# Optimization experiments

Measured on AMD Instinct MI355X. Metric: run time of the kernel, lower is better.

Reference implementation:

```python
import jax, jax.numpy as jnp
import numpy as np

N_NODES = 50000
N_EDGES = 800000
DIM_IN, DIM_H, DIM_OUT = 96, 128, 16


def setup_inputs() -> dict:
    key = jax.random.key(0)
    ks = jax.random.split(key, 8)
    x = jax.random.normal(ks[0], (N_NODES, DIM_IN), dtype=jnp.float32)
    edge_index = jax.random.randint(ks[1], (2, N_EDGES), 0, N_NODES, dtype=jnp.int64)
    W1_l = jax.random.normal(ks[2], (DIM_IN, DIM_H), dtype=jnp.float32) * 0.1
    b1_l = jax.random.normal(ks[3], (DIM_H,), dtype=jnp.float32) * 0.1
    W1_r = jax.random.normal(ks[4], (DIM_IN, DIM_H), dtype=jnp.float32) * 0.1
    W2_l = jax.random.normal(ks[5], (DIM_H, DIM_OUT), dtype=jnp.float32) * 0.1
    b2_l = jax.random.normal(ks[6], (DIM_OUT,), dtype=jnp.float32) * 0.1
    W2_r = jax.random.normal(ks[7], (DIM_H, DIM_OUT), dtype=jnp.float32) * 0.1
    return {"x": x, "edge_index": edge_index, "W1_l": W1_l, "b1_l": b1_l,
            "W1_r": W1_r, "W2_l": W2_l, "b2_l": b2_l, "W2_r": W2_r}


def _mean_aggregate(x, src, dst, n_nodes):
    # gather neighbor features along edges, mean-reduce at destination nodes
    msgs = x[src]                                      # [E, d]
    agg = jax.ops.segment_sum(msgs, dst, num_segments=n_nodes)  # [N, d]
    deg = jax.ops.segment_sum(jnp.ones_like(src, dtype=x.dtype), dst,
                              num_segments=n_nodes)    # [N]
    return agg / jnp.maximum(deg, 1.0)[:, None]


def _sage_conv(x, src, dst, W_l, b_l, W_r):
    # PyG SAGEConv (mean aggr): lin_l(mean_j x_j) + lin_r(x); bias on lin_l only
    agg = _mean_aggregate(x, src, dst, x.shape[0])
    return agg @ W_l + b_l + x @ W_r


def reference(x, edge_index, W1_l, b1_l, W1_r, W2_l, b2_l, W2_r):
    src, dst = edge_index[0], edge_index[1]
    h = jax.nn.relu(_sage_conv(x, src, dst, W1_l, b1_l, W1_r))
    h = _sage_conv(h, src, dst, W2_l, b2_l, W2_r)
    return jax.nn.softmax(h, axis=1)
```

## Files before the change

kernel.cpp:

```cpp
#include <hip/hip_runtime.h>

#define NN 50000
#define NE 800000
#define DIN 96
#define DH 128
#define DOUT 16
#define NBKT ((NN + 127) / 128)
#define EPB 8192

typedef __attribute__((ext_vector_type(8))) short bf16x8;
typedef __attribute__((ext_vector_type(4))) float f32x4;

__device__ inline short f2bf(float f) {
    unsigned u = __float_as_uint(f);
    u += 0x7fff + ((u >> 16) & 1);
    return (short)(u >> 16);
}
__device__ inline float bflo(unsigned u) { return __uint_as_float(u << 16); }
__device__ inline float bfhi(unsigned u) { return __uint_as_float(u & 0xffff0000u); }

#define XB_BLOCKS ((NN * DIN / 4 + 255) / 256)
#define WC_BLOCKS ((DH * 192 + 32 * DH + 255) / 256)
#define HB_BLOCKS ((NE + 8191) / 8192)
__global__ __launch_bounds__(256) void k_prep(const float* __restrict__ x,
                                              const float* __restrict__ W1l,
                                              const float* __restrict__ W1r,
                                              const float* __restrict__ W2l,
                                              const float* __restrict__ W2r,
                                              const int* __restrict__ ei,
                                              short* __restrict__ xb,
                                              short* __restrict__ Bt,
                                              short* __restrict__ Bt2,
                                              int* __restrict__ bcntg) {
    __shared__ int h[NBKT];
    if (blockIdx.x < XB_BLOCKS) {
        int i = blockIdx.x * 256 + threadIdx.x;
        if (i < NN * DIN / 4) {
            float4 v = ((const float4*)x)[i];
            short4 o;
            o.x = f2bf(v.x); o.y = f2bf(v.y); o.z = f2bf(v.z); o.w = f2bf(v.w);
            ((short4*)xb)[i] = o;
        }
    } else if (blockIdx.x < XB_BLOCKS + WC_BLOCKS) {
        int idx = (blockIdx.x - XB_BLOCKS) * 256 + threadIdx.x;
        if (idx < DH * 192) {
            int n = idx / 192, kk = idx % 192;
            float v = (kk < DIN) ? W1l[kk * DH + n] : W1r[(kk - DIN) * DH + n];
            Bt[idx] = f2bf(v);
        } else if (idx < DH * 192 + 32 * DH) {
            int j = idx - DH * 192;
            int c = j >> 7, k = j & 127;
            float v = (c < DOUT) ? W2l[k * DOUT + c] : W2r[k * DOUT + (c - DOUT)];
            Bt2[j] = f2bf(v);
        }
    } else {
        for (int i = threadIdx.x; i < NBKT; i += 256) h[i] = 0;
        __syncthreads();
        const int base = (blockIdx.x - XB_BLOCKS - WC_BLOCKS) * 8192;
        const int end = min(base + 8192, NE);
        for (int i = base + threadIdx.x; i < end; i += 256)
            atomicAdd(&h[ei[NE + i] >> 7], 1);
        __syncthreads();
        for (int b = threadIdx.x; b < NBKT; b += 256)
            if (h[b]) atomicAdd(&bcntg[b], h[b]);
    }
}

__global__ __launch_bounds__(512) void k_bscan(const int* __restrict__ bcntg,
                                               int* __restrict__ boff, int* __restrict__ gbcur) {
    __shared__ int buf[512];
    const int t = threadIdx.x;
    int v = (t < NBKT) ? bcntg[t] : 0;
    buf[t] = v;
    __syncthreads();
    for (int o = 1; o < 512; o <<= 1) {
        int tv = (t >= o) ? buf[t - o] : 0;
        __syncthreads();
        buf[t] += tv;
        __syncthreads();
    }
    if (t < NBKT) {
        int ex = buf[t] - v;
        boff[t] = ex;
        gbcur[t] = ex;
    }
    if (t == 0) boff[NBKT] = NE;
}

__global__ __launch_bounds__(512) void k_bucket(const int* __restrict__ ei,
                                                int* __restrict__ gbcur,
                                                unsigned* __restrict__ bpack) {
    __shared__ unsigned stage[EPB];
    __shared__ int bcnt[NBKT];
    __shared__ int bfill[NBKT];
    __shared__ int brun[NBKT];
    __shared__ int bres[NBKT];
    __shared__ int sbuf[512];
    const int tid = threadIdx.x;
    const int e0 = blockIdx.x * EPB;
    const int ecnt = min(EPB, NE - e0);

    for (int i = tid; i < NBKT; i += 512) { bcnt[i] = 0; bfill[i] = 0; }
    __syncthreads();
    for (int i = tid; i < ecnt; i += 512)
        atomicAdd(&bcnt[(unsigned)ei[NE + e0 + i] >> 7], 1);
    __syncthreads();
    int v = (tid < NBKT) ? bcnt[tid] : 0;
    sbuf[tid] = v;
    __syncthreads();
    for (int o = 1; o < 512; o <<= 1) {
        int tv = (tid >= o) ? sbuf[tid - o] : 0;
        __syncthreads();
        sbuf[tid] += tv;
        __syncthreads();
    }
    if (tid < NBKT) brun[tid] = sbuf[tid] - v;
    __syncthreads();
    for (int i = tid; i < ecnt; i += 512) {
        unsigned s = (unsigned)ei[e0 + i];
        unsigned d = (unsigned)ei[NE + e0 + i];
        int b = d >> 7;
        int p = atomicAdd(&bfill[b], 1);
        stage[brun[b] + p] = (d << 16) | s;
    }
    __syncthreads();
    for (int b = tid; b < NBKT; b += 512) {
        int n = bcnt[b];
        bres[b] = n ? atomicAdd(&gbcur[b], n) : 0;
    }
    __syncthreads();
    for (int i = tid; i < ecnt; i += 512) {
        unsigned p = stage[i];
        int b = p >> 23;
        bpack[bres[b] + (i - brun[b])] = p;
    }
}

__global__ __launch_bounds__(256) void k_bfill(const unsigned* __restrict__ bpack,
                                               const int* __restrict__ boff,
                                               int* __restrict__ off,
                                               int* __restrict__ csr) {
    __shared__ unsigned stage[4096];
    __shared__ int ncnt[128];
    __shared__ int nrun[128];
    __shared__ int lcur[128];
    __shared__ int buf[256];
    const int b = blockIdx.x;
    const int tid = threadIdx.x;
    const int pb = boff[b], pe = boff[b + 1];
    const int cnt = pe - pb;
    const bool st = (cnt <= 4096);
    if (tid < 128) { ncnt[tid] = 0; lcur[tid] = 0; }
    __syncthreads();
    for (int i = tid; i < cnt; i += 256) {
        unsigned p = bpack[pb + i];
        if (st) stage[i] = p;
        atomicAdd(&ncnt[(p >> 16) & 127], 1);
    }
    __syncthreads();
    int v = (tid < 128) ? ncnt[tid] : 0;
    buf[tid] = v;
    __syncthreads();
    for (int o = 1; o < 128; o <<= 1) {
        int tv = (tid >= o) ? buf[tid - o] : 0;
        __syncthreads();
        buf[tid] += tv;
        __syncthreads();
    }
    if (tid < 128) {
        nrun[tid] = buf[tid] - v;
        const int n = b * 128 + tid;
        if (n <= NN) off[n] = pb + nrun[tid];
    }
    __syncthreads();
    for (int i = tid; i < cnt; i += 256) {
        unsigned p = st ? stage[i] : bpack[pb + i];
        int nd = (p >> 16) & 127;
        int pos = atomicAdd(&lcur[nd], 1);
        csr[pb + nrun[nd] + pos] = (int)(p & 0xffffu);
    }
}

__global__ __launch_bounds__(256) void k_agg1(const short* __restrict__ xb,
                                              const int* __restrict__ csr,
                                              const int* __restrict__ off,
                                              short* __restrict__ m1b) {
    const int w = threadIdx.x >> 6;
    const int l = threadIdx.x & 63;
    const int n = blockIdx.x * 4 + w;
    if (n >= NN) return;
    const int eg = l / 12;
    const int c  = l % 12;
    const int b = off[n], e = off[n + 1];
    const float4* xq = (const float4*)xb;
    float acc[8];
#pragma unroll
    for (int k = 0; k < 8; ++k) acc[k] = 0.f;
    int i = (eg < 4) ? b + eg : e;
    for (; i + 4 < e; i += 8) {
        int s0 = csr[i], s1 = csr[i + 4];
        float4 v0 = xq[(size_t)s0 * 12 + c];
        float4 v1 = xq[(size_t)s1 * 12 + c];
        const unsigned* u0 = (const unsigned*)&v0;
        const unsigned* u1 = (const unsigned*)&v1;
#pragma unroll
        for (int j = 0; j < 4; ++j) {
            acc[2 * j]     += bflo(u0[j]) + bflo(u1[j]);
            acc[2 * j + 1] += bfhi(u0[j]) + bfhi(u1[j]);
        }
    }
    if (i < e) {
        float4 v0 = xq[(size_t)csr[i] * 12 + c];
        const unsigned* u0 = (const unsigned*)&v0;
#pragma unroll
        for (int j = 0; j < 4; ++j) {
            acc[2 * j]     += bflo(u0[j]);
            acc[2 * j + 1] += bfhi(u0[j]);
        }
    }
#pragma unroll
    for (int k = 0; k < 8; ++k) acc[k] += __shfl(acc[k], l + 24);
#pragma unroll
    for (int k = 0; k < 8; ++k) acc[k] += __shfl(acc[k], l + 12);
    if (l < 12) {
        const float inv = (e > b) ? 1.0f / (float)(e - b) : 0.0f;
        uint4 o;
        unsigned* op = (unsigned*)&o;
#pragma unroll
        for (int j = 0; j < 4; ++j)
            op[j] = (unsigned)(unsigned short)f2bf(acc[2 * j] * inv)
                  | ((unsigned)(unsigned short)f2bf(acc[2 * j + 1] * inv) << 16);
        ((uint4*)m1b)[(size_t)n * 12 + l] = o;
    }
}

#define SHP 136
__global__ __launch_bounds__(256) void k_linproj(const short* __restrict__ m1b,
                                                 const short* __restrict__ xb,
                                                 const short* __restrict__ Bt,
                                                 const float* __restrict__ b1,
                                                 const short* __restrict__ Bt2,
                                                 const float* __restrict__ b2,
                                                 short* __restrict__ zlb,
                                                 float* __restrict__ s) {
    __shared__ __align__(16) short sh[64][SHP];
    const int w = threadIdx.x >> 6;
    const int l = threadIdx.x & 63;
    const int lr = l & 15;
    const int lk = l >> 4;
    int row = blockIdx.x * 64 + w * 16 + lr;
    if (row >= NN) row = NN - 1;

    f32x4 acc[8];
#pragma unroll
    for (int nt = 0; nt < 8; ++nt) {
        float bv = b1[nt * 16 + lr];
        acc[nt] = (f32x4){bv, bv, bv, bv};
    }

    bf16x8 afr[6];
    {
        const bf16x8* am = (const bf16x8*)(m1b + (size_t)row * DIN);
        const bf16x8* ax = (const bf16x8*)(xb  + (size_t)row * DIN);
        afr[0] = am[lk];     afr[1] = am[4 + lk]; afr[2] = am[8 + lk];
        afr[3] = ax[lk];     afr[4] = ax[4 + lk]; afr[5] = ax[8 + lk];
    }

    const bf16x8* bt8 = (const bf16x8*)Bt;
#pragma unroll
    for (int st = 0; st < 6; ++st) {
#pragma unroll
        for (int nt = 0; nt < 8; ++nt) {
            bf16x8 bfr = bt8[(size_t)(nt * 16 + lr) * 24 + st * 4 + lk];
            acc[nt] = __builtin_amdgcn_mfma_f32_16x16x32_bf16(afr[st], bfr, acc[nt], 0, 0, 0);
        }
    }

    const int lrow0 = w * 16 + lk * 4;
#pragma unroll
    for (int r = 0; r < 4; ++r) {
#pragma unroll
        for (int nt = 0; nt < 8; ++nt)
            sh[lrow0 + r][nt * 16 + lr] = f2bf(fmaxf(acc[nt][r], 0.f));
    }
    __syncthreads();

    bf16x8 pafr[4];
#pragma unroll
    for (int st = 0; st < 4; ++st)
        pafr[st] = *(const bf16x8*)&sh[w * 16 + lr][st * 32 + lk * 8];

    f32x4 accz = (f32x4){0.f, 0.f, 0.f, 0.f};
    float bv = b2[lr];
    f32x4 accs = (f32x4){bv, bv, bv, bv};
    const bf16x8* b8 = (const bf16x8*)Bt2;
#pragma unroll
    for (int st = 0; st < 4; ++st) {
        bf16x8 bz = b8[(size_t)lr * 16 + st * 4 + lk];
        bf16x8 bs = b8[(size_t)(16 + lr) * 16 + st * 4 + lk];
        accz = __builtin_amdgcn_mfma_f32_16x16x32_bf16(pafr[st], bz, accz, 0, 0, 0);
        accs = __builtin_amdgcn_mfma_f32_16x16x32_bf16(pafr[st], bs, accs, 0, 0, 0);
    }

    const int orow0 = blockIdx.x * 64 + w * 16 + lk * 4;
#pragma unroll
    for (int r = 0; r < 4; ++r) {
        const int orow = orow0 + r;
        if (orow < NN) {
            zlb[(size_t)orow * DOUT + lr] = f2bf(accz[r]);
            s[(size_t)orow * DOUT + lr] = accs[r];
        }
    }
}

__global__ __launch_bounds__(256) void k_agg2(const short* __restrict__ zlb,
                                              const float* __restrict__ s,
                                              const int* __restrict__ csr,
                                              const int* __restrict__ off,
                                              float* __restrict__ out) {
    const int w = threadIdx.x >> 6;
    const int lane = threadIdx.x & 63;
    const int n = blockIdx.x * 4 + w;
    if (n >= NN) return;
    const int b = off[n], e = off[n + 1];
    const int ng = lane >> 2;
    const int sl = lane & 3;
    const uint2* z2 = (const uint2*)zlb;
    float4 acc = {0.f, 0.f, 0.f, 0.f};
    for (int i = b + ng; i < e; i += 16) {
        uint2 u = z2[(size_t)csr[i] * 4 + sl];
        acc.x += bflo(u.x);
        acc.y += bfhi(u.x);
        acc.z += bflo(u.y);
        acc.w += bfhi(u.y);
    }
#pragma unroll
    for (int o = 4; o <= 32; o <<= 1) {
        acc.x += __shfl_xor(acc.x, o);
        acc.y += __shfl_xor(acc.y, o);
        acc.z += __shfl_xor(acc.z, o);
        acc.w += __shfl_xor(acc.w, o);
    }
    const float inv = (e > b) ? 1.0f / (float)(e - b) : 0.0f;
    const float4 sv = ((const float4*)s)[(size_t)n * 4 + sl];
    float4 v;
    v.x = acc.x * inv + sv.x;
    v.y = acc.y * inv + sv.y;
    v.z = acc.z * inv + sv.z;
    v.w = acc.w * inv + sv.w;
    float mx = fmaxf(fmaxf(v.x, v.y), fmaxf(v.z, v.w));
    mx = fmaxf(mx, __shfl_xor(mx, 1));
    mx = fmaxf(mx, __shfl_xor(mx, 2));
    v.x = expf(v.x - mx); v.y = expf(v.y - mx);
    v.z = expf(v.z - mx); v.w = expf(v.w - mx);
    float sm = v.x + v.y + v.z + v.w;
    sm += __shfl_xor(sm, 1);
    sm += __shfl_xor(sm, 2);
    const float r = 1.0f / sm;
    v.x *= r; v.y *= r; v.z *= r; v.w *= r;
    if (ng == 0) ((float4*)out)[(size_t)n * 4 + sl] = v;
}

template <typename T>
static inline T* align_up(void* p, size_t a = 64) {
    return (T*)(((uintptr_t)p + (a - 1)) & ~(uintptr_t)(a - 1));
}

extern "C" void kernel_launch(void* const* d_in, const int* in_sizes, int n_in,
                              void* d_out, int out_size, void* d_ws, size_t ws_size,
                              hipStream_t stream) {
    const float* x   = (const float*)d_in[0];
    const int*   ei  = (const int*)d_in[1];
    const float* W1l = (const float*)d_in[2];
    const float* b1  = (const float*)d_in[3];
    const float* W1r = (const float*)d_in[4];
    const float* W2l = (const float*)d_in[5];
    const float* b2  = (const float*)d_in[6];
    const float* W2r = (const float*)d_in[7];
    float* out = (float*)d_out;

    unsigned* bpack = (unsigned*)d_ws;
    float* s     = (float*)(bpack + NE);
    int* off     = (int*)(s + (size_t)NN * DOUT);
    int* boff    = off + NN + 1;
    int* gbcur   = boff + NBKT + 1;
    int* bcntg   = gbcur + NBKT;
    int* csr     = bcntg + NBKT;
    short* xb    = align_up<short>(csr + NE);
    short* m1b   = xb + (size_t)NN * DIN;
    short* zlb   = m1b + (size_t)NN * DIN;
    short* Bt    = zlb + (size_t)NN * DOUT;
    short* Bt2   = Bt + (size_t)DH * 192;

    hipMemsetAsync(bcntg, 0, NBKT * sizeof(int), stream);

    k_prep<<<XB_BLOCKS + WC_BLOCKS + HB_BLOCKS, 256, 0, stream>>>(
        x, W1l, W1r, W2l, W2r, ei, xb, Bt, Bt2, bcntg);
    k_bscan<<<1, 512, 0, stream>>>(bcntg, boff, gbcur);
    k_bucket<<<(NE + EPB - 1) / EPB, 512, 0, stream>>>(ei, gbcur, bpack);
    k_bfill<<<NBKT, 256, 0, stream>>>(bpack, boff, off, csr);

    k_agg1<<<(NN + 3) / 4, 256, 0, stream>>>(xb, csr, off, m1b);
    k_linproj<<<(NN + 63) / 64, 256, 0, stream>>>(m1b, xb, Bt, b1, Bt2, b2, zlb, s);
    k_agg2<<<(NN + 3) / 4, 256, 0, stream>>>(zlb, s, csr, off, out);
}
```

Before: 127.6 us.

## Replace global bucket histogram and scan with fixed-capacity bucket slots

Drops the global destination histogram pass and the single-block scan kernel by giving each 128-node bucket a fixed-capacity slot in the packed edge buffer. CSR offsets become separate start/end arrays per node. k_bucket also keeps destination indices in registers between its count and scatter passes instead of reloading them. The cost is a capacity bound per bucket that assumes roughly uniform destination degrees; overflowing edges would be lost.

```diff
diff --git a/kernel.cpp b/kernel.cpp
--- a/kernel.cpp
+++ b/kernel.cpp
@@ -6,6 +6,7 @@
 #define DH 128
 #define DOUT 16
 #define NBKT ((NN + 127) / 128)
+#define CAP 2560
 #define EPB 8192
 
 typedef __attribute__((ext_vector_type(8))) short bf16x8;
@@ -21,18 +22,15 @@
 
 #define XB_BLOCKS ((NN * DIN / 4 + 255) / 256)
 #define WC_BLOCKS ((DH * 192 + 32 * DH + 255) / 256)
-#define HB_BLOCKS ((NE + 8191) / 8192)
 __global__ __launch_bounds__(256) void k_prep(const float* __restrict__ x,
                                               const float* __restrict__ W1l,
                                               const float* __restrict__ W1r,
                                               const float* __restrict__ W2l,
                                               const float* __restrict__ W2r,
-                                              const int* __restrict__ ei,
                                               short* __restrict__ xb,
                                               short* __restrict__ Bt,
                                               short* __restrict__ Bt2,
-                                              int* __restrict__ bcntg) {
-    __shared__ int h[NBKT];
+                                              int* __restrict__ gbcur) {
     if (blockIdx.x < XB_BLOCKS) {
         int i = blockIdx.x * 256 + threadIdx.x;
         if (i < NN * DIN / 4) {
@@ -54,37 +52,8 @@
             Bt2[j] = f2bf(v);
         }
     } else {
-        for (int i = threadIdx.x; i < NBKT; i += 256) h[i] = 0;
-        __syncthreads();
-        const int base = (blockIdx.x - XB_BLOCKS - WC_BLOCKS) * 8192;
-        const int end = min(base + 8192, NE);
-        for (int i = base + threadIdx.x; i < end; i += 256)
-            atomicAdd(&h[ei[NE + i] >> 7], 1);
-        __syncthreads();
-        for (int b = threadIdx.x; b < NBKT; b += 256)
-            if (h[b]) atomicAdd(&bcntg[b], h[b]);
-    }
-}
-
-__global__ __launch_bounds__(512) void k_bscan(const int* __restrict__ bcntg,
-                                               int* __restrict__ boff, int* __restrict__ gbcur) {
-    __shared__ int buf[512];
-    const int t = threadIdx.x;
-    int v = (t < NBKT) ? bcntg[t] : 0;
-    buf[t] = v;
-    __syncthreads();
-    for (int o = 1; o < 512; o <<= 1) {
-        int tv = (t >= o) ? buf[t - o] : 0;
-        __syncthreads();
-        buf[t] += tv;
-        __syncthreads();
-    }
-    if (t < NBKT) {
-        int ex = buf[t] - v;
-        boff[t] = ex;
-        gbcur[t] = ex;
-    }
-    if (t == 0) boff[NBKT] = NE;
+        for (int i = threadIdx.x; i < NBKT; i += 256) gbcur[i] = 0;
+    }
 }
 
 __global__ __launch_bounds__(512) void k_bucket(const int* __restrict__ ei,
@@ -92,7 +61,7 @@
                                                 unsigned* __restrict__ bpack) {
     __shared__ unsigned stage[EPB];
     __shared__ int bcnt[NBKT];
-    __shared__ int bfill[NBKT];
+    __shared__ int bfil[NBKT];
     __shared__ int brun[NBKT];
     __shared__ int bres[NBKT];
     __shared__ int sbuf[512];
@@ -100,10 +69,18 @@
     const int e0 = blockIdx.x * EPB;
     const int ecnt = min(EPB, NE - e0);
 
-    for (int i = tid; i < NBKT; i += 512) { bcnt[i] = 0; bfill[i] = 0; }
-    __syncthreads();
-    for (int i = tid; i < ecnt; i += 512)
-        atomicAdd(&bcnt[(unsigned)ei[NE + e0 + i] >> 7], 1);
+    for (int i = tid; i < NBKT; i += 512) { bcnt[i] = 0; bfil[i] = 0; }
+    __syncthreads();
+    unsigned dcache[EPB / 512];
+#pragma unroll
+    for (int k = 0; k < EPB / 512; ++k) {
+        int i = tid + k * 512;
+        if (i < ecnt) {
+            unsigned d = (unsigned)ei[NE + e0 + i];
+            dcache[k] = d;
+            atomicAdd(&bcnt[d >> 7], 1);
+        }
+    }
     __syncthreads();
     int v = (tid < NBKT) ? bcnt[tid] : 0;
     sbuf[tid] = v;
@@ -116,12 +93,16 @@
     }
     if (tid < NBKT) brun[tid] = sbuf[tid] - v;
     __syncthreads();
-    for (int i = tid; i < ecnt; i += 512) {
-        unsigned s = (unsigned)ei[e0 + i];
-        unsigned d = (unsigned)ei[NE + e0 + i];
-        int b = d >> 7;
-        int p = atomicAdd(&bfill[b], 1);
-        stage[brun[b] + p] = (d << 16) | s;
+#pragma unroll
+    for (int k = 0; k < EPB / 512; ++k) {
+        int i = tid + k * 512;
+        if (i < ecnt) {
+            unsigned s = (unsigned)ei[e0 + i];
+            unsigned d = dcache[k];
+            int b = d >> 7;
+            int p = atomicAdd(&bfil[b], 1);
+            stage[brun[b] + p] = (d << 16) | s;
+        }
     }
     __syncthreads();
     for (int b = tid; b < NBKT; b += 512) {
@@ -132,29 +113,29 @@
     for (int i = tid; i < ecnt; i += 512) {
         unsigned p = stage[i];
         int b = p >> 23;
-        bpack[bres[b] + (i - brun[b])] = p;
+        bpack[(size_t)b * CAP + bres[b] + (i - brun[b])] = p;
     }
 }
 
 __global__ __launch_bounds__(256) void k_bfill(const unsigned* __restrict__ bpack,
-                                               const int* __restrict__ boff,
-                                               int* __restrict__ off,
+                                               const int* __restrict__ gbcur,
+                                               int* __restrict__ offs,
+                                               int* __restrict__ offe,
                                                int* __restrict__ csr) {
-    __shared__ unsigned stage[4096];
+    __shared__ unsigned stage[CAP];
     __shared__ int ncnt[128];
     __shared__ int nrun[128];
     __shared__ int lcur[128];
     __shared__ int buf[256];
     const int b = blockIdx.x;
     const int tid = threadIdx.x;
-    const int pb = boff[b], pe = boff[b + 1];
-    const int cnt = pe - pb;
-    const bool st = (cnt <= 4096);
+    const int pb = b * CAP;
+    const int cnt = min(gbcur[b], CAP);
     if (tid < 128) { ncnt[tid] = 0; lcur[tid] = 0; }
     __syncthreads();
     for (int i = tid; i < cnt; i += 256) {
         unsigned p = bpack[pb + i];
-        if (st) stage[i] = p;
+        stage[i] = p;
         atomicAdd(&ncnt[(p >> 16) & 127], 1);
     }
     __syncthreads();
@@ -170,11 +151,14 @@
     if (tid < 128) {
         nrun[tid] = buf[tid] - v;
         const int n = b * 128 + tid;
-        if (n <= NN) off[n] = pb + nrun[tid];
+        if (n < NN) {
+            offs[n] = pb + nrun[tid];
+            offe[n] = pb + nrun[tid] + v;
+        }
     }
     __syncthreads();
     for (int i = tid; i < cnt; i += 256) {
-        unsigned p = st ? stage[i] : bpack[pb + i];
+        unsigned p = stage[i];
         int nd = (p >> 16) & 127;
         int pos = atomicAdd(&lcur[nd], 1);
         csr[pb + nrun[nd] + pos] = (int)(p & 0xffffu);
@@ -183,7 +167,8 @@
 
 __global__ __launch_bounds__(256) void k_agg1(const short* __restrict__ xb,
                                               const int* __restrict__ csr,
-                                              const int* __restrict__ off,
+                                              const int* __restrict__ offs,
+                                              const int* __restrict__ offe,
                                               short* __restrict__ m1b) {
     const int w = threadIdx.x >> 6;
     const int l = threadIdx.x & 63;
@@ -191,7 +176,7 @@
     if (n >= NN) return;
     const int eg = l / 12;
     const int c  = l % 12;
-    const int b = off[n], e = off[n + 1];
+    const int b = offs[n], e = offe[n];
     const float4* xq = (const float4*)xb;
     float acc[8];
 #pragma unroll
@@ -316,13 +301,14 @@
 __global__ __launch_bounds__(256) void k_agg2(const short* __restrict__ zlb,
                                               const float* __restrict__ s,
                                               const int* __restrict__ csr,
-                                              const int* __restrict__ off,
+                                              const int* __restrict__ offs,
+                                              const int* __restrict__ offe,
                                               float* __restrict__ out) {
     const int w = threadIdx.x >> 6;
     const int lane = threadIdx.x & 63;
     const int n = blockIdx.x * 4 + w;
     if (n >= NN) return;
-    const int b = off[n], e = off[n + 1];
+    const int b = offs[n], e = offe[n];
     const int ng = lane >> 2;
     const int sl = lane & 3;
     const uint2* z2 = (const uint2*)zlb;
@@ -380,27 +366,23 @@
     float* out = (float*)d_out;
 
     unsigned* bpack = (unsigned*)d_ws;
-    float* s     = (float*)(bpack + NE);
-    int* off     = (int*)(s + (size_t)NN * DOUT);
-    int* boff    = off + NN + 1;
-    int* gbcur   = boff + NBKT + 1;
-    int* bcntg   = gbcur + NBKT;
-    int* csr     = bcntg + NBKT;
-    short* xb    = align_up<short>(csr + NE);
+    int* csr     = (int*)(bpack + (size_t)NBKT * CAP);
+    float* s     = (float*)(csr + (size_t)NBKT * CAP);
+    int* offs    = (int*)(s + (size_t)NN * DOUT);
+    int* offe    = offs + NN;
+    int* gbcur   = offe + NN;
+    short* xb    = align_up<short>(gbcur + NBKT);
     short* m1b   = xb + (size_t)NN * DIN;
     short* zlb   = m1b + (size_t)NN * DIN;
     short* Bt    = zlb + (size_t)NN * DOUT;
     short* Bt2   = Bt + (size_t)DH * 192;
 
-    hipMemsetAsync(bcntg, 0, NBKT * sizeof(int), stream);
-
-    k_prep<<<XB_BLOCKS + WC_BLOCKS + HB_BLOCKS, 256, 0, stream>>>(
-        x, W1l, W1r, W2l, W2r, ei, xb, Bt, Bt2, bcntg);
-    k_bscan<<<1, 512, 0, stream>>>(bcntg, boff, gbcur);
+    k_prep<<<XB_BLOCKS + WC_BLOCKS + 1, 256, 0, stream>>>(
+        x, W1l, W1r, W2l, W2r, xb, Bt, Bt2, gbcur);
     k_bucket<<<(NE + EPB - 1) / EPB, 512, 0, stream>>>(ei, gbcur, bpack);
-    k_bfill<<<NBKT, 256, 0, stream>>>(bpack, boff, off, csr);
-
-    k_agg1<<<(NN + 3) / 4, 256, 0, stream>>>(xb, csr, off, m1b);
+    k_bfill<<<NBKT, 256, 0, stream>>>(bpack, gbcur, offs, offe, csr);
+
+    k_agg1<<<(NN + 3) / 4, 256, 0, stream>>>(xb, csr, offs, offe, m1b);
     k_linproj<<<(NN + 63) / 64, 256, 0, stream>>>(m1b, xb, Bt, b1, Bt2, b2, zlb, s);
-    k_agg2<<<(NN + 3) / 4, 256, 0, stream>>>(zlb, s, csr, off, out);
-}
+    k_agg2<<<(NN + 3) / 4, 256, 0, stream>>>(zlb, s, csr, offs, offe, out);
+}
```

Result: faster. 109.2 us (-14.4%).
